# Kernel optimization log

Hardware: AMD Instinct MI355X
Metric: run time of the kernel (lower is better)

The kernel has to match this reference:

```python
import jax, jax.numpy as jnp
import numpy as np

N_NODES = 50000
N_EDGES = 600000
NODE_DIM = 128
HIDDEN = 128
LN_EPS = 1e-5


def setup_inputs() -> dict:
    key = jax.random.key(0)
    ks = jax.random.split(key, 12)
    x = jax.random.normal(ks[0], (N_NODES, NODE_DIM), dtype=jnp.float32)
    edge_index = jax.random.randint(ks[1], (2, N_EDGES), 0, N_NODES, dtype=jnp.int32)
    # GCNConv weights (glorot-ish scaling)
    W1 = jax.random.normal(ks[2], (NODE_DIM, HIDDEN), dtype=jnp.float32) / np.sqrt(NODE_DIM)
    b1 = jnp.zeros((HIDDEN,), jnp.float32)
    W2 = jax.random.normal(ks[3], (HIDDEN, HIDDEN), dtype=jnp.float32) / np.sqrt(HIDDEN)
    b2 = jnp.zeros((HIDDEN,), jnp.float32)
    g1 = jnp.ones((HIDDEN,), jnp.float32)
    beta1 = jnp.zeros((HIDDEN,), jnp.float32)
    g2 = jnp.ones((HIDDEN,), jnp.float32)
    beta2 = jnp.zeros((HIDDEN,), jnp.float32)
    return {"x": x, "edge_index": edge_index, "W1": W1, "b1": b1, "g1": g1,
            "beta1": beta1, "W2": W2, "b2": b2, "g2": g2, "beta2": beta2}


def _gcn_conv(x, src, dst, norm, W, b, n):
    # x' = sum_{j->i} norm_ji * (x_j @ W) + b   (self-loops already in src/dst)
    h = x @ W                                   # [N, H]
    msg = h[src] * norm[:, None]                # [E+N, H]
    out = jax.ops.segment_sum(msg, dst, num_segments=n)
    return out + b


def _layer_norm(x, gamma, beta):
    mu = jnp.mean(x, axis=-1, keepdims=True)
    var = jnp.mean((x - mu) ** 2, axis=-1, keepdims=True)
    return (x - mu) * jax.lax.rsqrt(var + LN_EPS) * gamma + beta


def reference(x, edge_index, W1, b1, g1, beta1, W2, b2, g2, beta2):
    n = x.shape[0]
    loop = jnp.arange(n, dtype=edge_index.dtype)
    src = jnp.concatenate([edge_index[0], loop])
    dst = jnp.concatenate([edge_index[1], loop])
    # symmetric normalization with self-loops (PyG GCNConv default)
    deg = jax.ops.segment_sum(jnp.ones_like(dst, dtype=x.dtype), dst, num_segments=n)
    dinv = jnp.where(deg > 0, jax.lax.rsqrt(jnp.maximum(deg, 1.0)), 0.0)
    norm = dinv[src] * dinv[dst]                # [E+N]

    h = _gcn_conv(x, src, dst, norm, W1, b1, n)
    h = _layer_norm(h, g1, beta1)
    h = jax.nn.relu(h)                          # relu between layers only
    h = _gcn_conv(h, src, dst, norm, W2, b2, n)
    h = _layer_norm(h, g2, beta2)
    return h
```

## Files before the change

kernel.cpp:

```cpp
#include <hip/hip_runtime.h>

#define DIM 128
#define LN_EPS 1e-5f

typedef __attribute__((ext_vector_type(8))) short bf16x8;
typedef __attribute__((ext_vector_type(4))) float f32x4;

static __device__ __forceinline__ unsigned short f2bf(float f) {
    unsigned int u = __builtin_bit_cast(unsigned int, f);
    u += 0x7fffu + ((u >> 16) & 1u);
    return (unsigned short)(u >> 16);
}
static __device__ __forceinline__ float bf2f_lo(unsigned int u) {
    return __builtin_bit_cast(float, u << 16);
}
static __device__ __forceinline__ float bf2f_hi(unsigned int u) {
    return __builtin_bit_cast(float, u & 0xffff0000u);
}

__global__ __launch_bounds__(256) void wt_count_kernel(const float* __restrict__ W1,
                                                       const float* __restrict__ W2,
                                                       unsigned short* __restrict__ Wt1,
                                                       unsigned short* __restrict__ Wt2,
                                                       const int* __restrict__ dst,
                                                       int* __restrict__ counts,
                                                       int* __restrict__ rank, int E) {
    int b = blockIdx.x;
    if (b < 128) {
        int elem = b * 256 + threadIdx.x;
        int which = elem >> 14;
        int rest = elem & 16383;
        int c = rest >> 7;
        int k = rest & 127;
        const float* W = which ? W2 : W1;
        unsigned short* Wt = which ? Wt2 : Wt1;
        Wt[c * 128 + k] = f2bf(W[k * 128 + c]);
    } else {
        int e = (b - 128) * 256 + threadIdx.x;
        if (e < E) {
            int r = atomicAdd(&counts[dst[e]], 1);
            rank[e] = r;
        }
    }
}

__global__ __launch_bounds__(256) void scan_fused_kernel(const int* __restrict__ counts,
                                                         int* __restrict__ bsums,
                                                         int* __restrict__ bpref,
                                                         int* __restrict__ sync2,
                                                         int* __restrict__ rowptr,
                                                         float* __restrict__ dinv,
                                                         int n, int E, int nb) {
    __shared__ int ts[256];
    int tid = threadIdx.x;
    int b = blockIdx.x;
    int base = b * 1024 + tid * 4;
    int v[4];
#pragma unroll
    for (int j = 0; j < 4; ++j) {
        int i = base + j;
        v[j] = (i < n) ? counts[i] : 0;
        if (i < n) dinv[i] = rsqrtf((float)(v[j] + 1));
    }
    int s = v[0] + v[1] + v[2] + v[3];
    ts[tid] = s;
    __syncthreads();
    for (int off = 1; off < 256; off <<= 1) {
        int t2 = (tid >= off) ? ts[tid - off] : 0;
        __syncthreads();
        ts[tid] += t2;
        __syncthreads();
    }
    int excl = ts[tid] - s;

    if (tid == 255) {
        bsums[b] = ts[255];
        __threadfence();
        int t = atomicAdd(&sync2[0], 1);
        if (t == nb - 1) {
            __threadfence();
            int acc = 0;
            for (int k = 0; k < nb; ++k) {
                int sv = bsums[k];
                bpref[k] = acc;
                acc += sv;
            }
            __threadfence();
            atomicExch(&sync2[1], 1);
        }
    }
    if (tid == 0) {
        while (atomicAdd(&sync2[1], 0) == 0) { __builtin_amdgcn_s_sleep(8); }
    }
    __syncthreads();
    __threadfence();

    int pre = bpref[b] + excl;
#pragma unroll
    for (int j = 0; j < 4; ++j) {
        int i = base + j;
        if (i < n) rowptr[i] = pre;
        pre += v[j];
    }
    if (b == 0 && tid == 0) rowptr[n] = E;
}

__global__ __launch_bounds__(256) void gemm1_fill_kernel(const float* __restrict__ A,
                                                         const unsigned short* __restrict__ Bt,
                                                         const float* __restrict__ dinv,
                                                         unsigned short* __restrict__ H,
                                                         int n, int ntiles, int gG,
                                                         const int* __restrict__ src,
                                                         const int* __restrict__ dst,
                                                         const int* __restrict__ rowptr,
                                                         const int* __restrict__ rank,
                                                         unsigned short* __restrict__ colsrc,
                                                         int E) {
    __shared__ unsigned short Wlds[128 * 136];
    if (blockIdx.x >= gG) {
        int e = (blockIdx.x - gG) * 256 + threadIdx.x;
        if (e < E) {
            int p = rowptr[dst[e]] + rank[e];
            colsrc[p] = (unsigned short)src[e];
        }
        return;
    }
    for (int u = threadIdx.x; u < 2048; u += 256) {
        int row = u >> 4;
        int sub = u & 15;
        *(bf16x8*)&Wlds[row * 136 + sub * 8] = *(const bf16x8*)(Bt + row * 128 + sub * 8);
    }
    __syncthreads();

    int wid = threadIdx.x >> 6;
    int lane = threadIdx.x & 63;
    int tile = blockIdx.x * 4 + wid;
    if (tile >= ntiles) tile = ntiles - 1;
    int r0 = tile * 16;
    int mrow = lane & 15;
    int kgrp = lane >> 4;

    int arow_i = r0 + mrow;
    if (arow_i > n - 1) arow_i = n - 1;
    const float* arow = A + (size_t)arow_i * DIM + kgrp * 8;

    f32x4 acc[8];
#pragma unroll
    for (int t = 0; t < 8; ++t) acc[t] = (f32x4){0.f, 0.f, 0.f, 0.f};

#pragma unroll
    for (int kc = 0; kc < 4; ++kc) {
        float4 v0 = *(const float4*)(arow + kc * 32);
        float4 v1 = *(const float4*)(arow + kc * 32 + 4);
        bf16x8 af;
        af[0] = (short)f2bf(v0.x); af[1] = (short)f2bf(v0.y);
        af[2] = (short)f2bf(v0.z); af[3] = (short)f2bf(v0.w);
        af[4] = (short)f2bf(v1.x); af[5] = (short)f2bf(v1.y);
        af[6] = (short)f2bf(v1.z); af[7] = (short)f2bf(v1.w);
#pragma unroll
        for (int t = 0; t < 8; ++t) {
            bf16x8 bfv = *(const bf16x8*)&Wlds[(t * 16 + mrow) * 136 + kc * 32 + kgrp * 8];
            acc[t] = __builtin_amdgcn_mfma_f32_16x16x32_bf16(af, bfv, acc[t], 0, 0, 0);
        }
    }

    float dv[4];
#pragma unroll
    for (int reg = 0; reg < 4; ++reg) {
        int rr = r0 + kgrp * 4 + reg;
        dv[reg] = (rr < n) ? dinv[rr] : 0.f;
    }

    __syncthreads();

    unsigned short* Wst = &Wlds[wid * 16 * 136];
#pragma unroll
    for (int t = 0; t < 8; ++t) {
#pragma unroll
        for (int reg = 0; reg < 4; ++reg) {
            Wst[(kgrp * 4 + reg) * 136 + t * 16 + mrow] = f2bf(acc[t][reg] * dv[reg]);
        }
    }

#pragma unroll
    for (int q = 0; q < 4; ++q) {
        int e = q * 64 + lane;
        int row = e >> 4;
        int c16 = e & 15;
        int grow = r0 + row;
        if (grow < n) {
            *(bf16x8*)&H[(size_t)grow * DIM + c16 * 8] = *(const bf16x8*)&Wst[row * 136 + c16 * 8];
        }
    }
}

__global__ __launch_bounds__(128, 5) void gather_gemm_kernel(const int* __restrict__ rowptr,
                                                             const unsigned short* __restrict__ colsrc,
                                                             const uint4* __restrict__ H4,
                                                             const float* __restrict__ dinv,
                                                             const float* __restrict__ bias,
                                                             const float* __restrict__ gamma,
                                                             const float* __restrict__ beta,
                                                             const unsigned short* __restrict__ Wt2,
                                                             unsigned short* __restrict__ H2,
                                                             int n) {
    __shared__ unsigned short Tl[16][136];
    int wid = threadIdx.x >> 6;
    int lane = threadIdx.x & 63;
    int r0 = blockIdx.x * 16;
    int grp = lane >> 4;
    int gl = lane & 15;

#pragma unroll
    for (int t = 0; t < 2; ++t) {
        int r = r0 + wid * 8 + t * 4 + grp;
        int rc = (r < n) ? r : (n - 1);
        float di = dinv[rc];
        uint4 su = H4[(size_t)rc * 16 + gl];
        int p0 = rowptr[rc];
        int p1 = rowptr[rc + 1];
        float a0 = bf2f_lo(su.x), a1 = bf2f_hi(su.x);
        float a2 = bf2f_lo(su.y), a3 = bf2f_hi(su.y);
        float a4 = bf2f_lo(su.z), a5 = bf2f_hi(su.z);
        float a6 = bf2f_lo(su.w), a7 = bf2f_hi(su.w);

        int deg = p1 - p0;
        int m = max(deg, __shfl_xor(deg, 16));
        m = max(m, __shfl_xor(m, 32));
        int nch = (m + 15) >> 4;

        for (int c = 0; c < nch; ++c) {
            int cb = c * 16;
            int gi = p0 + cb + gl;
            gi = gi < p1 ? gi : p1 - 1;
            int idxv = (int)colsrc[gi];

            uint4 h[16];
#pragma unroll
            for (int j = 0; j < 16; ++j) {
                int sS = __shfl(idxv, grp * 16 + j);
                h[j] = H4[(size_t)sS * 16 + gl];
            }
#pragma unroll
            for (int j = 0; j < 16; ++j) {
                bool act = (cb + j < deg);
                a0 += act ? bf2f_lo(h[j].x) : 0.f;
                a1 += act ? bf2f_hi(h[j].x) : 0.f;
                a2 += act ? bf2f_lo(h[j].y) : 0.f;
                a3 += act ? bf2f_hi(h[j].y) : 0.f;
                a4 += act ? bf2f_lo(h[j].z) : 0.f;
                a5 += act ? bf2f_hi(h[j].z) : 0.f;
                a6 += act ? bf2f_lo(h[j].w) : 0.f;
                a7 += act ? bf2f_hi(h[j].w) : 0.f;
            }
        }

        float4 bb0 = ((const float4*)bias)[gl * 2];
        float4 bb1 = ((const float4*)bias)[gl * 2 + 1];
        float v0 = a0 * di + bb0.x;
        float v1 = a1 * di + bb0.y;
        float v2 = a2 * di + bb0.z;
        float v3 = a3 * di + bb0.w;
        float v4 = a4 * di + bb1.x;
        float v5 = a5 * di + bb1.y;
        float v6 = a6 * di + bb1.z;
        float v7 = a7 * di + bb1.w;

        float s1 = v0 + v1 + v2 + v3 + v4 + v5 + v6 + v7;
        float s2 = v0 * v0 + v1 * v1 + v2 * v2 + v3 * v3 +
                   v4 * v4 + v5 * v5 + v6 * v6 + v7 * v7;
#pragma unroll
        for (int off = 8; off > 0; off >>= 1) {
            s1 += __shfl_xor(s1, off);
            s2 += __shfl_xor(s2, off);
        }
        float mu = s1 * (1.f / 128.f);
        float var = s2 * (1.f / 128.f) - mu * mu;
        float rstd = rsqrtf(var + LN_EPS);

        float4 gg0 = ((const float4*)gamma)[gl * 2];
        float4 gg1 = ((const float4*)gamma)[gl * 2 + 1];
        float4 be0 = ((const float4*)beta)[gl * 2];
        float4 be1 = ((const float4*)beta)[gl * 2 + 1];

        float o0 = fmaxf((v0 - mu) * rstd * gg0.x + be0.x, 0.f);
        float o1 = fmaxf((v1 - mu) * rstd * gg0.y + be0.y, 0.f);
        float o2 = fmaxf((v2 - mu) * rstd * gg0.z + be0.z, 0.f);
        float o3 = fmaxf((v3 - mu) * rstd * gg0.w + be0.w, 0.f);
        float o4 = fmaxf((v4 - mu) * rstd * gg1.x + be1.x, 0.f);
        float o5 = fmaxf((v5 - mu) * rstd * gg1.y + be1.y, 0.f);
        float o6 = fmaxf((v6 - mu) * rstd * gg1.z + be1.z, 0.f);
        float o7 = fmaxf((v7 - mu) * rstd * gg1.w + be1.w, 0.f);

        bf16x8 pk;
        pk[0] = (short)f2bf(o0); pk[1] = (short)f2bf(o1);
        pk[2] = (short)f2bf(o2); pk[3] = (short)f2bf(o3);
        pk[4] = (short)f2bf(o4); pk[5] = (short)f2bf(o5);
        pk[6] = (short)f2bf(o6); pk[7] = (short)f2bf(o7);
        *(bf16x8*)&Tl[wid * 8 + t * 4 + grp][gl * 8] = pk;
    }

    __syncthreads();

    int mrow = lane & 15;
    int kg = lane >> 4;
    f32x4 acc[4];
#pragma unroll
    for (int tt = 0; tt < 4; ++tt) acc[tt] = (f32x4){0.f, 0.f, 0.f, 0.f};

#pragma unroll
    for (int kc = 0; kc < 4; ++kc) {
        bf16x8 af = *(const bf16x8*)&Tl[mrow][kc * 32 + kg * 8];
#pragma unroll
        for (int tt = 0; tt < 4; ++tt) {
            int trow = (wid * 4 + tt) * 16 + mrow;
            bf16x8 bv = *(const bf16x8*)(Wt2 + (size_t)trow * 128 + kc * 32 + kg * 8);
            acc[tt] = __builtin_amdgcn_mfma_f32_16x16x32_bf16(af, bv, acc[tt], 0, 0, 0);
        }
    }

    float dv[4];
#pragma unroll
    for (int reg = 0; reg < 4; ++reg) {
        int rr = r0 + kg * 4 + reg;
        dv[reg] = (rr < n) ? dinv[rr] : 0.f;
    }

    __syncthreads();

#pragma unroll
    for (int tt = 0; tt < 4; ++tt) {
#pragma unroll
        for (int reg = 0; reg < 4; ++reg) {
            Tl[kg * 4 + reg][(wid * 4 + tt) * 16 + mrow] = f2bf(acc[tt][reg] * dv[reg]);
        }
    }
    __syncthreads();

#pragma unroll
    for (int q = 0; q < 2; ++q) {
        int e = q * 128 + threadIdx.x;
        int row = e >> 4;
        int c16 = e & 15;
        int grow = r0 + row;
        if (grow < n) {
            *(bf16x8*)&H2[(size_t)grow * DIM + c16 * 8] = *(const bf16x8*)&Tl[row][c16 * 8];
        }
    }
}

__global__ __launch_bounds__(256, 5) void gather_out_kernel(const int* __restrict__ rowptr,
                                                            const unsigned short* __restrict__ colsrc,
                                                            const uint4* __restrict__ H4,
                                                            const float* __restrict__ dinv,
                                                            const float* __restrict__ bias,
                                                            const float* __restrict__ gamma,
                                                            const float* __restrict__ beta,
                                                            float* __restrict__ out,
                                                            int n) {
    int wid = threadIdx.x >> 6;
    int lane = threadIdx.x & 63;
    int grp = lane >> 4;
    int gl = lane & 15;
    int r = blockIdx.x * 16 + wid * 4 + grp;
    int valid = (r < n);
    int rc = valid ? r : (n - 1);

    float di = dinv[rc];
    uint4 su = H4[(size_t)rc * 16 + gl];
    int p0 = rowptr[rc];
    int p1 = rowptr[rc + 1];
    float a0 = bf2f_lo(su.x), a1 = bf2f_hi(su.x);
    float a2 = bf2f_lo(su.y), a3 = bf2f_hi(su.y);
    float a4 = bf2f_lo(su.z), a5 = bf2f_hi(su.z);
    float a6 = bf2f_lo(su.w), a7 = bf2f_hi(su.w);

    int deg = p1 - p0;
    int m = max(deg, __shfl_xor(deg, 16));
    m = max(m, __shfl_xor(m, 32));
    int nch = (m + 15) >> 4;

    for (int c = 0; c < nch; ++c) {
        int cb = c * 16;
        int gi = p0 + cb + gl;
        gi = gi < p1 ? gi : p1 - 1;
        int idxv = (int)colsrc[gi];

        uint4 h[16];
#pragma unroll
        for (int j = 0; j < 16; ++j) {
            int sS = __shfl(idxv, grp * 16 + j);
            h[j] = H4[(size_t)sS * 16 + gl];
        }
#pragma unroll
        for (int j = 0; j < 16; ++j) {
            bool act = (cb + j < deg);
            a0 += act ? bf2f_lo(h[j].x) : 0.f;
            a1 += act ? bf2f_hi(h[j].x) : 0.f;
            a2 += act ? bf2f_lo(h[j].y) : 0.f;
            a3 += act ? bf2f_hi(h[j].y) : 0.f;
            a4 += act ? bf2f_lo(h[j].z) : 0.f;
            a5 += act ? bf2f_hi(h[j].z) : 0.f;
            a6 += act ? bf2f_lo(h[j].w) : 0.f;
            a7 += act ? bf2f_hi(h[j].w) : 0.f;
        }
    }

    float4 bb0 = ((const float4*)bias)[gl * 2];
    float4 bb1 = ((const float4*)bias)[gl * 2 + 1];
    float v0 = a0 * di + bb0.x;
    float v1 = a1 * di + bb0.y;
    float v2 = a2 * di + bb0.z;
    float v3 = a3 * di + bb0.w;
    float v4 = a4 * di + bb1.x;
    float v5 = a5 * di + bb1.y;
    float v6 = a6 * di + bb1.z;
    float v7 = a7 * di + bb1.w;

    float s1 = v0 + v1 + v2 + v3 + v4 + v5 + v6 + v7;
    float s2 = v0 * v0 + v1 * v1 + v2 * v2 + v3 * v3 +
               v4 * v4 + v5 * v5 + v6 * v6 + v7 * v7;
#pragma unroll
    for (int off = 8; off > 0; off >>= 1) {
        s1 += __shfl_xor(s1, off);
        s2 += __shfl_xor(s2, off);
    }
    float mu = s1 * (1.f / 128.f);
    float var = s2 * (1.f / 128.f) - mu * mu;
    float rstd = rsqrtf(var + LN_EPS);

    float4 gg0 = ((const float4*)gamma)[gl * 2];
    float4 gg1 = ((const float4*)gamma)[gl * 2 + 1];
    float4 be0 = ((const float4*)beta)[gl * 2];
    float4 be1 = ((const float4*)beta)[gl * 2 + 1];

    float o0 = (v0 - mu) * rstd * gg0.x + be0.x;
    float o1 = (v1 - mu) * rstd * gg0.y + be0.y;
    float o2 = (v2 - mu) * rstd * gg0.z + be0.z;
    float o3 = (v3 - mu) * rstd * gg0.w + be0.w;
    float o4 = (v4 - mu) * rstd * gg1.x + be1.x;
    float o5 = (v5 - mu) * rstd * gg1.y + be1.y;
    float o6 = (v6 - mu) * rstd * gg1.z + be1.z;
    float o7 = (v7 - mu) * rstd * gg1.w + be1.w;

    if (valid) {
        ((float4*)out)[(size_t)r * 32 + gl * 2] = make_float4(o0, o1, o2, o3);
        ((float4*)out)[(size_t)r * 32 + gl * 2 + 1] = make_float4(o4, o5, o6, o7);
    }
}

extern "C" void kernel_launch(void* const* d_in, const int* in_sizes, int n_in,
                              void* d_out, int out_size, void* d_ws, size_t ws_size,
                              hipStream_t stream) {
    const float* x   = (const float*)d_in[0];
    const int*   ei  = (const int*)d_in[1];
    const float* W1  = (const float*)d_in[2];
    const float* b1  = (const float*)d_in[3];
    const float* g1  = (const float*)d_in[4];
    const float* be1 = (const float*)d_in[5];
    const float* W2  = (const float*)d_in[6];
    const float* b2  = (const float*)d_in[7];
    const float* g2  = (const float*)d_in[8];
    const float* be2 = (const float*)d_in[9];

    int n = in_sizes[0] / DIM;
    int E = in_sizes[1] / 2;
    const int* src = ei;
    const int* dst = ei + E;

    char* wp = (char*)d_ws;
    auto alloc = [&](size_t bytes) {
        void* p = (void*)wp;
        wp += (bytes + 255) & ~(size_t)255;
        return p;
    };
    float*          dinv   = (float*)alloc((size_t)n * 4);
    int*            counts = (int*)alloc((size_t)(n + 64) * 4);
    int*            sync2  = counts + n;
    int*            rowptr = (int*)alloc((size_t)(n + 1) * 4);
    int*            rank   = (int*)alloc((size_t)E * 4);
    int*            bsums  = (int*)alloc(256 * 4);
    int*            bpref  = (int*)alloc(256 * 4);
    unsigned short* colsrc = (unsigned short*)alloc((size_t)E * 2);
    unsigned short* Wt1    = (unsigned short*)alloc(128 * 128 * 2);
    unsigned short* Wt2    = (unsigned short*)alloc(128 * 128 * 2);
    unsigned short* H      = (unsigned short*)alloc((size_t)n * DIM * 2);
    unsigned short* H2     = (unsigned short*)alloc((size_t)n * DIM * 2);

    hipMemsetAsync(counts, 0, (size_t)(n + 64) * 4, stream);

    int gE = (E + 255) / 256;
    wt_count_kernel<<<128 + gE, 256, 0, stream>>>(W1, W2, Wt1, Wt2, dst, counts, rank, E);

    int nb1 = (n + 1023) / 1024;
    scan_fused_kernel<<<nb1, 256, 0, stream>>>(counts, bsums, bpref, sync2,
                                               rowptr, dinv, n, E, nb1);

    int ntiles = (n + 15) / 16;
    int gG = (ntiles + 3) / 4;

    gemm1_fill_kernel<<<gG + gE, 256, 0, stream>>>(x, Wt1, dinv, H, n, ntiles, gG,
                                                   src, dst, rowptr, rank, colsrc, E);

    gather_gemm_kernel<<<ntiles, 128, 0, stream>>>(rowptr, colsrc, (const uint4*)H, dinv,
                                                   b1, g1, be1, Wt2, H2, n);

    gather_out_kernel<<<ntiles, 256, 0, stream>>>(rowptr, colsrc, (const uint4*)H2, dinv,
                                                  b2, g2, be2, (float*)d_out, n);
}
```

Before: 217.1 us.

## Widen gather-GEMM blocks, prefetch next neighbor indices, use nontemporal stores

gather_gemm_kernel now runs 256 threads per block. Each wave aggregates one 4-row group instead of looping over two, and the MFMA stage is split so each wave computes two output column tiles. Both gather kernels prefetch the next chunk's neighbor indices before issuing the current chunk's row loads, to hide index-load latency. H and H2 writes use nontemporal stores, and launch bounds drop to 3 blocks per CU, which may change register allocation and occupancy.

```diff
diff --git a/kernel.cpp b/kernel.cpp
--- a/kernel.cpp
+++ b/kernel.cpp
@@ -5,6 +5,7 @@
 
 typedef __attribute__((ext_vector_type(8))) short bf16x8;
 typedef __attribute__((ext_vector_type(4))) float f32x4;
+typedef __attribute__((ext_vector_type(4))) unsigned int u32x4;
 
 static __device__ __forceinline__ unsigned short f2bf(float f) {
     unsigned int u = __builtin_bit_cast(unsigned int, f);
@@ -16,6 +17,9 @@
 }
 static __device__ __forceinline__ float bf2f_hi(unsigned int u) {
     return __builtin_bit_cast(float, u & 0xffff0000u);
+}
+static __device__ __forceinline__ void nt_store16(void* p, bf16x8 v) {
+    __builtin_nontemporal_store(__builtin_bit_cast(u32x4, v), (u32x4*)p);
 }
 
 __global__ __launch_bounds__(256) void wt_count_kernel(const float* __restrict__ W1,
@@ -189,12 +193,12 @@
         int c16 = e & 15;
         int grow = r0 + row;
         if (grow < n) {
-            *(bf16x8*)&H[(size_t)grow * DIM + c16 * 8] = *(const bf16x8*)&Wst[row * 136 + c16 * 8];
-        }
-    }
-}
-
-__global__ __launch_bounds__(128, 5) void gather_gemm_kernel(const int* __restrict__ rowptr,
+            nt_store16(&H[(size_t)grow * DIM + c16 * 8], *(const bf16x8*)&Wst[row * 136 + c16 * 8]);
+        }
+    }
+}
+
+__global__ __launch_bounds__(256, 3) void gather_gemm_kernel(const int* __restrict__ rowptr,
                                                              const unsigned short* __restrict__ colsrc,
                                                              const uint4* __restrict__ H4,
                                                              const float* __restrict__ dinv,
@@ -211,109 +215,116 @@
     int grp = lane >> 4;
     int gl = lane & 15;
 
-#pragma unroll
-    for (int t = 0; t < 2; ++t) {
-        int r = r0 + wid * 8 + t * 4 + grp;
-        int rc = (r < n) ? r : (n - 1);
-        float di = dinv[rc];
-        uint4 su = H4[(size_t)rc * 16 + gl];
-        int p0 = rowptr[rc];
-        int p1 = rowptr[rc + 1];
-        float a0 = bf2f_lo(su.x), a1 = bf2f_hi(su.x);
-        float a2 = bf2f_lo(su.y), a3 = bf2f_hi(su.y);
-        float a4 = bf2f_lo(su.z), a5 = bf2f_hi(su.z);
-        float a6 = bf2f_lo(su.w), a7 = bf2f_hi(su.w);
-
-        int deg = p1 - p0;
-        int m = max(deg, __shfl_xor(deg, 16));
-        m = max(m, __shfl_xor(m, 32));
-        int nch = (m + 15) >> 4;
-
-        for (int c = 0; c < nch; ++c) {
-            int cb = c * 16;
-            int gi = p0 + cb + gl;
-            gi = gi < p1 ? gi : p1 - 1;
-            int idxv = (int)colsrc[gi];
-
-            uint4 h[16];
-#pragma unroll
-            for (int j = 0; j < 16; ++j) {
-                int sS = __shfl(idxv, grp * 16 + j);
-                h[j] = H4[(size_t)sS * 16 + gl];
-            }
-#pragma unroll
-            for (int j = 0; j < 16; ++j) {
-                bool act = (cb + j < deg);
-                a0 += act ? bf2f_lo(h[j].x) : 0.f;
-                a1 += act ? bf2f_hi(h[j].x) : 0.f;
-                a2 += act ? bf2f_lo(h[j].y) : 0.f;
-                a3 += act ? bf2f_hi(h[j].y) : 0.f;
-                a4 += act ? bf2f_lo(h[j].z) : 0.f;
-                a5 += act ? bf2f_hi(h[j].z) : 0.f;
-                a6 += act ? bf2f_lo(h[j].w) : 0.f;
-                a7 += act ? bf2f_hi(h[j].w) : 0.f;
-            }
-        }
-
-        float4 bb0 = ((const float4*)bias)[gl * 2];
-        float4 bb1 = ((const float4*)bias)[gl * 2 + 1];
-        float v0 = a0 * di + bb0.x;
-        float v1 = a1 * di + bb0.y;
-        float v2 = a2 * di + bb0.z;
-        float v3 = a3 * di + bb0.w;
-        float v4 = a4 * di + bb1.x;
-        float v5 = a5 * di + bb1.y;
-        float v6 = a6 * di + bb1.z;
-        float v7 = a7 * di + bb1.w;
-
-        float s1 = v0 + v1 + v2 + v3 + v4 + v5 + v6 + v7;
-        float s2 = v0 * v0 + v1 * v1 + v2 * v2 + v3 * v3 +
-                   v4 * v4 + v5 * v5 + v6 * v6 + v7 * v7;
-#pragma unroll
-        for (int off = 8; off > 0; off >>= 1) {
-            s1 += __shfl_xor(s1, off);
-            s2 += __shfl_xor(s2, off);
-        }
-        float mu = s1 * (1.f / 128.f);
-        float var = s2 * (1.f / 128.f) - mu * mu;
-        float rstd = rsqrtf(var + LN_EPS);
-
-        float4 gg0 = ((const float4*)gamma)[gl * 2];
-        float4 gg1 = ((const float4*)gamma)[gl * 2 + 1];
-        float4 be0 = ((const float4*)beta)[gl * 2];
-        float4 be1 = ((const float4*)beta)[gl * 2 + 1];
-
-        float o0 = fmaxf((v0 - mu) * rstd * gg0.x + be0.x, 0.f);
-        float o1 = fmaxf((v1 - mu) * rstd * gg0.y + be0.y, 0.f);
-        float o2 = fmaxf((v2 - mu) * rstd * gg0.z + be0.z, 0.f);
-        float o3 = fmaxf((v3 - mu) * rstd * gg0.w + be0.w, 0.f);
-        float o4 = fmaxf((v4 - mu) * rstd * gg1.x + be1.x, 0.f);
-        float o5 = fmaxf((v5 - mu) * rstd * gg1.y + be1.y, 0.f);
-        float o6 = fmaxf((v6 - mu) * rstd * gg1.z + be1.z, 0.f);
-        float o7 = fmaxf((v7 - mu) * rstd * gg1.w + be1.w, 0.f);
-
-        bf16x8 pk;
-        pk[0] = (short)f2bf(o0); pk[1] = (short)f2bf(o1);
-        pk[2] = (short)f2bf(o2); pk[3] = (short)f2bf(o3);
-        pk[4] = (short)f2bf(o4); pk[5] = (short)f2bf(o5);
-        pk[6] = (short)f2bf(o6); pk[7] = (short)f2bf(o7);
-        *(bf16x8*)&Tl[wid * 8 + t * 4 + grp][gl * 8] = pk;
-    }
+    int r = r0 + wid * 4 + grp;
+    int rc = (r < n) ? r : (n - 1);
+    float di = dinv[rc];
+    uint4 su = H4[(size_t)rc * 16 + gl];
+    int p0 = rowptr[rc];
+    int p1 = rowptr[rc + 1];
+    float a0 = bf2f_lo(su.x), a1 = bf2f_hi(su.x);
+    float a2 = bf2f_lo(su.y), a3 = bf2f_hi(su.y);
+    float a4 = bf2f_lo(su.z), a5 = bf2f_hi(su.z);
+    float a6 = bf2f_lo(su.w), a7 = bf2f_hi(su.w);
+
+    int deg = p1 - p0;
+    int m = max(deg, __shfl_xor(deg, 16));
+    m = max(m, __shfl_xor(m, 32));
+    int nch = (m + 15) >> 4;
+
+    int idxv = 0;
+    if (nch > 0) {
+        int gi = p0 + gl;
+        gi = gi < p1 ? gi : p1 - 1;
+        idxv = (int)colsrc[gi];
+    }
+    for (int c = 0; c < nch; ++c) {
+        int cb = c * 16;
+        int idxn = idxv;
+        if (c + 1 < nch) {
+            int gi2 = p0 + cb + 16 + gl;
+            gi2 = gi2 < p1 ? gi2 : p1 - 1;
+            idxn = (int)colsrc[gi2];
+        }
+
+        uint4 h[16];
+#pragma unroll
+        for (int j = 0; j < 16; ++j) {
+            int sS = __shfl(idxv, grp * 16 + j);
+            h[j] = H4[(size_t)sS * 16 + gl];
+        }
+#pragma unroll
+        for (int j = 0; j < 16; ++j) {
+            bool act = (cb + j < deg);
+            a0 += act ? bf2f_lo(h[j].x) : 0.f;
+            a1 += act ? bf2f_hi(h[j].x) : 0.f;
+            a2 += act ? bf2f_lo(h[j].y) : 0.f;
+            a3 += act ? bf2f_hi(h[j].y) : 0.f;
+            a4 += act ? bf2f_lo(h[j].z) : 0.f;
+            a5 += act ? bf2f_hi(h[j].z) : 0.f;
+            a6 += act ? bf2f_lo(h[j].w) : 0.f;
+            a7 += act ? bf2f_hi(h[j].w) : 0.f;
+        }
+        idxv = idxn;
+    }
+
+    float4 bb0 = ((const float4*)bias)[gl * 2];
+    float4 bb1 = ((const float4*)bias)[gl * 2 + 1];
+    float v0 = a0 * di + bb0.x;
+    float v1 = a1 * di + bb0.y;
+    float v2 = a2 * di + bb0.z;
+    float v3 = a3 * di + bb0.w;
+    float v4 = a4 * di + bb1.x;
+    float v5 = a5 * di + bb1.y;
+    float v6 = a6 * di + bb1.z;
+    float v7 = a7 * di + bb1.w;
+
+    float s1 = v0 + v1 + v2 + v3 + v4 + v5 + v6 + v7;
+    float s2 = v0 * v0 + v1 * v1 + v2 * v2 + v3 * v3 +
+               v4 * v4 + v5 * v5 + v6 * v6 + v7 * v7;
+#pragma unroll
+    for (int off = 8; off > 0; off >>= 1) {
+        s1 += __shfl_xor(s1, off);
+        s2 += __shfl_xor(s2, off);
+    }
+    float mu = s1 * (1.f / 128.f);
+    float var = s2 * (1.f / 128.f) - mu * mu;
+    float rstd = rsqrtf(var + LN_EPS);
+
+    float4 gg0 = ((const float4*)gamma)[gl * 2];
+    float4 gg1 = ((const float4*)gamma)[gl * 2 + 1];
+    float4 be0 = ((const float4*)beta)[gl * 2];
+    float4 be1 = ((const float4*)beta)[gl * 2 + 1];
+
+    float o0 = fmaxf((v0 - mu) * rstd * gg0.x + be0.x, 0.f);
+    float o1 = fmaxf((v1 - mu) * rstd * gg0.y + be0.y, 0.f);
+    float o2 = fmaxf((v2 - mu) * rstd * gg0.z + be0.z, 0.f);
+    float o3 = fmaxf((v3 - mu) * rstd * gg0.w + be0.w, 0.f);
+    float o4 = fmaxf((v4 - mu) * rstd * gg1.x + be1.x, 0.f);
+    float o5 = fmaxf((v5 - mu) * rstd * gg1.y + be1.y, 0.f);
+    float o6 = fmaxf((v6 - mu) * rstd * gg1.z + be1.z, 0.f);
+    float o7 = fmaxf((v7 - mu) * rstd * gg1.w + be1.w, 0.f);
+
+    bf16x8 pk;
+    pk[0] = (short)f2bf(o0); pk[1] = (short)f2bf(o1);
+    pk[2] = (short)f2bf(o2); pk[3] = (short)f2bf(o3);
+    pk[4] = (short)f2bf(o4); pk[5] = (short)f2bf(o5);
+    pk[6] = (short)f2bf(o6); pk[7] = (short)f2bf(o7);
+    *(bf16x8*)&Tl[wid * 4 + grp][gl * 8] = pk;
 
     __syncthreads();
 
     int mrow = lane & 15;
     int kg = lane >> 4;
-    f32x4 acc[4];
-#pragma unroll
-    for (int tt = 0; tt < 4; ++tt) acc[tt] = (f32x4){0.f, 0.f, 0.f, 0.f};
+    f32x4 acc[2];
+    acc[0] = (f32x4){0.f, 0.f, 0.f, 0.f};
+    acc[1] = (f32x4){0.f, 0.f, 0.f, 0.f};
 
 #pragma unroll
     for (int kc = 0; kc < 4; ++kc) {
         bf16x8 af = *(const bf16x8*)&Tl[mrow][kc * 32 + kg * 8];
 #pragma unroll
-        for (int tt = 0; tt < 4; ++tt) {
-            int trow = (wid * 4 + tt) * 16 + mrow;
+        for (int tt = 0; tt < 2; ++tt) {
+            int trow = (wid * 2 + tt) * 16 + mrow;
             bf16x8 bv = *(const bf16x8*)(Wt2 + (size_t)trow * 128 + kc * 32 + kg * 8);
             acc[tt] = __builtin_amdgcn_mfma_f32_16x16x32_bf16(af, bv, acc[tt], 0, 0, 0);
         }
@@ -329,27 +340,26 @@
     __syncthreads();
 
 #pragma unroll
-    for (int tt = 0; tt < 4; ++tt) {
+    for (int tt = 0; tt < 2; ++tt) {
 #pragma unroll
         for (int reg = 0; reg < 4; ++reg) {
-            Tl[kg * 4 + reg][(wid * 4 + tt) * 16 + mrow] = f2bf(acc[tt][reg] * dv[reg]);
-        }
-    }
-    __syncthreads();
-
-#pragma unroll
-    for (int q = 0; q < 2; ++q) {
-        int e = q * 128 + threadIdx.x;
+            Tl[kg * 4 + reg][(wid * 2 + tt) * 16 + mrow] = f2bf(acc[tt][reg] * dv[reg]);
+        }
+    }
+    __syncthreads();
+
+    {
+        int e = threadIdx.x;
         int row = e >> 4;
         int c16 = e & 15;
         int grow = r0 + row;
         if (grow < n) {
-            *(bf16x8*)&H2[(size_t)grow * DIM + c16 * 8] = *(const bf16x8*)&Tl[row][c16 * 8];
-        }
-    }
-}
-
-__global__ __launch_bounds__(256, 5) void gather_out_kernel(const int* __restrict__ rowptr,
+            nt_store16(&H2[(size_t)grow * DIM + c16 * 8], *(const bf16x8*)&Tl[row][c16 * 8]);
+        }
+    }
+}
+
+__global__ __launch_bounds__(256, 3) void gather_out_kernel(const int* __restrict__ rowptr,
                                                             const unsigned short* __restrict__ colsrc,
                                                             const uint4* __restrict__ H4,
                                                             const float* __restrict__ dinv,
@@ -380,11 +390,20 @@
     m = max(m, __shfl_xor(m, 32));
     int nch = (m + 15) >> 4;
 
+    int idxv = 0;
+    if (nch > 0) {
+        int gi = p0 + gl;
+        gi = gi < p1 ? gi : p1 - 1;
+        idxv = (int)colsrc[gi];
+    }
     for (int c = 0; c < nch; ++c) {
         int cb = c * 16;
-        int gi = p0 + cb + gl;
-        gi = gi < p1 ? gi : p1 - 1;
-        int idxv = (int)colsrc[gi];
+        int idxn = idxv;
+        if (c + 1 < nch) {
+            int gi2 = p0 + cb + 16 + gl;
+            gi2 = gi2 < p1 ? gi2 : p1 - 1;
+            idxn = (int)colsrc[gi2];
+        }
 
         uint4 h[16];
 #pragma unroll
@@ -404,6 +423,7 @@
             a6 += act ? bf2f_lo(h[j].w) : 0.f;
             a7 += act ? bf2f_hi(h[j].w) : 0.f;
         }
+        idxv = idxn;
     }
 
     float4 bb0 = ((const float4*)bias)[gl * 2];
@@ -502,7 +522,7 @@
     gemm1_fill_kernel<<<gG + gE, 256, 0, stream>>>(x, Wt1, dinv, H, n, ntiles, gG,
                                                    src, dst, rowptr, rank, colsrc, E);
 
-    gather_gemm_kernel<<<ntiles, 128, 0, stream>>>(rowptr, colsrc, (const uint4*)H, dinv,
+    gather_gemm_kernel<<<ntiles, 256, 0, stream>>>(rowptr, colsrc, (const uint4*)H, dinv,
                                                    b1, g1, be1, Wt2, H2, n);
 
     gather_out_kernel<<<ntiles, 256, 0, stream>>>(rowptr, colsrc, (const uint4*)H2, dinv,
```

After: 203.8 us. -6.1%, faster.
